# Optimization experiments

Hardware: AMD Instinct MI355X
Metric: run time of the kernel (lower is better)

Reference implementation:

```python
import jax, jax.numpy as jnp
import numpy as np

B, S, H, T = 64, 512, 768, 3


def setup_inputs() -> dict:
    key = jax.random.key(0)
    ks = jax.random.split(key, 8)
    hidden = jax.random.normal(ks[0], (B, S, H), dtype=jnp.float32)
    labels = jax.random.randint(ks[1], (B, S), 0, T, dtype=jnp.int32)
    # variable-length attention mask; torchcrf requires mask[:, 0] all on
    lengths = jax.random.randint(ks[2], (B,), S // 4, S + 1, dtype=jnp.int32)
    mask = (jnp.arange(S)[None, :] < lengths[:, None]).astype(jnp.int32)
    W = jax.random.normal(ks[3], (H, T), dtype=jnp.float32) * 0.02
    b = jax.random.normal(ks[4], (T,), dtype=jnp.float32) * 0.02
    transitions = jax.random.normal(ks[5], (T, T), dtype=jnp.float32) * 0.1
    start_trans = jax.random.normal(ks[6], (T,), dtype=jnp.float32) * 0.1
    end_trans = jax.random.normal(ks[7], (T,), dtype=jnp.float32) * 0.1
    return {"hidden": hidden, "labels": labels, "mask": mask, "W": W, "b": b,
            "transitions": transitions, "start_trans": start_trans, "end_trans": end_trans}


def _crf_nll(emissions, tags, mask, trans, start, end):
    # emissions: (B,S,T) float; tags/mask: (B,S) int. Returns sum NLL (scalar).
    mask_f = mask.astype(emissions.dtype)
    bidx = jnp.arange(emissions.shape[0])
    # --- numerator: score of the given tag path ---
    first_tag = tags[:, 0]
    num = start[first_tag] + emissions[bidx, 0, first_tag]
    prev, cur = tags[:, :-1], tags[:, 1:]
    step = trans[prev, cur] + jnp.take_along_axis(emissions[:, 1:], cur[..., None], axis=2)[..., 0]
    num = num + jnp.sum(step * mask_f[:, 1:], axis=1)
    lengths = jnp.sum(mask, axis=1)
    last_tag = jnp.take_along_axis(tags, (lengths - 1)[:, None], axis=1)[:, 0]
    num = num + end[last_tag]
    # --- denominator: log-partition via forward algorithm (lax.scan) ---
    alpha0 = start[None, :] + emissions[:, 0]  # (B,T)
    def fwd_step(alpha, inp):
        e, m = inp  # e: (B,T), m: (B,)
        nxt = jax.scipy.special.logsumexp(alpha[:, :, None] + trans[None] + e[:, None, :], axis=1)
        return jnp.where(m[:, None] > 0, nxt, alpha), None
    emis_t = jnp.swapaxes(emissions[:, 1:], 0, 1)  # (S-1,B,T)
    mask_t = jnp.swapaxes(mask[:, 1:], 0, 1)       # (S-1,B)
    alpha, _ = jax.lax.scan(fwd_step, alpha0, (emis_t, mask_t))
    logZ = jax.scipy.special.logsumexp(alpha + end[None, :], axis=1)
    return jnp.sum(logZ - num)


def reference(hidden, labels, mask, W, b, transitions, start_trans, end_trans):
    # classifier: Linear + ReLU -> emissions (B,S,T)
    emissions = jax.nn.relu(jnp.einsum("bsh,ht->bst", hidden, W) + b)
    negloglike = _crf_nll(emissions, labels, mask, transitions, start_trans, end_trans)
    return emissions, negloglike
```

## Files before the change

### kernel.cpp

```cpp
#include <hip/hip_runtime.h>
#include <math.h>

#define NB 64
#define NS 512
#define NH 768
#define NT 3
#define EMIS_N (NB * NS * NT)
#define NEGINF (-1e30f)
#define PSTRIDE 12
#define BPB 32

__device__ __forceinline__ float lse3(float a, float b, float c) {
    float m = fmaxf(fmaxf(a, b), c);
    return m + __logf(__expf(a - m) + __expf(b - m) + __expf(c - m));
}

__global__ __launch_bounds__(256) void emis_crf_kernel(
    const float* __restrict__ hidden,
    const int*   __restrict__ labels,
    const int*   __restrict__ mask,
    const float* __restrict__ W,
    const float* __restrict__ bias,
    const float* __restrict__ trans,
    const float* __restrict__ startv,
    float* __restrict__ out,
    float* __restrict__ ws)
{
    __shared__ float sP[4][12];

    const int tid  = threadIdx.x;
    const int lane = tid & 63;
    const int wv   = tid >> 6;
    const int wid  = blockIdx.x * 4 + wv;
    const int sub  = lane & 15;
    const int rsel = lane >> 4;
    const int row  = wid * 4 + rsel;
    const int b    = row >> 9;
    const int p    = row & (NS - 1);

    if (blockIdx.x == 0 && tid == 0) out[EMIS_N] = 0.0f;

    const int* lrow = labels + b * NS;
    const int* mrow = mask   + b * NS;
    int mk = 0, labc = 0, labp = 0;
    if (sub == 0) {
        mk   = mrow[p];
        labc = lrow[p];
        labp = lrow[p - (p > 0 ? 1 : 0)];
    }

    const float* hrow = hidden + (size_t)row * NH;
    float a0 = 0.f, a1 = 0.f, a2 = 0.f;
    #pragma unroll
    for (int it = 0; it < 12; ++it) {
        const int h0 = it * 64 + sub * 4;
        const float4 x  = *reinterpret_cast<const float4*>(hrow + h0);
        const float4 q0 = *reinterpret_cast<const float4*>(W + h0 * 3);
        const float4 q1 = *reinterpret_cast<const float4*>(W + h0 * 3 + 4);
        const float4 q2 = *reinterpret_cast<const float4*>(W + h0 * 3 + 8);
        a0 = fmaf(x.x, q0.x, a0); a1 = fmaf(x.x, q0.y, a1); a2 = fmaf(x.x, q0.z, a2);
        a0 = fmaf(x.y, q0.w, a0); a1 = fmaf(x.y, q1.x, a1); a2 = fmaf(x.y, q1.y, a2);
        a0 = fmaf(x.z, q1.z, a0); a1 = fmaf(x.z, q1.w, a1); a2 = fmaf(x.z, q2.x, a2);
        a0 = fmaf(x.w, q2.y, a0); a1 = fmaf(x.w, q2.z, a1); a2 = fmaf(x.w, q2.w, a2);
    }
    #pragma unroll
    for (int d = 8; d; d >>= 1) {
        a0 += __shfl_xor(a0, d);
        a1 += __shfl_xor(a1, d);
        a2 += __shfl_xor(a2, d);
    }

    const float e0 = fmaxf(a0 + bias[0], 0.f);
    const float e1 = fmaxf(a1 + bias[1], 0.f);
    const float e2 = fmaxf(a2 + bias[2], 0.f);

    if (sub < 3) out[row * NT + sub] = (sub == 0) ? e0 : (sub == 1) ? e1 : e2;

    float term = 0.f;
    if (sub == 0) {
        const float esel = (labc == 0) ? e0 : (labc == 1) ? e1 : e2;
        if (p == 0) {
            term = startv[labc] + esel;
        } else if (mk) {
            term = trans[labp * 3 + labc] + esel;
        }
    }

    const int il = (lane < 9) ? (lane / 3) : 0;
    const int jl = (lane < 9) ? (lane % 3) : 0;
    const float tc0 = trans[jl], tc1 = trans[3 + jl], tc2 = trans[6 + jl];
    float Pv = (il == jl) ? 0.f : NEGINF;

    const int pbase = p & ~3;
    #pragma unroll
    for (int k = 0; k < 4; ++k) {
        const int src = k << 4;
        const float ee0 = __shfl(e0, src);
        const float ee1 = __shfl(e1, src);
        const float ee2 = __shfl(e2, src);
        const int   mm  = __shfl(mk, src);
        const float Pi0 = __shfl(Pv, il * 3 + 0);
        const float Pi1 = __shfl(Pv, il * 3 + 1);
        const float Pi2 = __shfl(Pv, il * 3 + 2);
        const float ej  = (jl == 0) ? ee0 : (jl == 1) ? ee1 : ee2;
        const float q   = lse3(Pi0 + tc0, Pi1 + tc1, Pi2 + tc2) + ej;
        const bool act  = ((pbase + k) >= 1) && (mm != 0);
        Pv = act ? q : Pv;
    }

    const float np = __shfl(term, 0) + __shfl(term, 16) +
                     __shfl(term, 32) + __shfl(term, 48);

    if (lane < 9)  sP[wv][lane] = Pv;
    if (lane == 0) sP[wv][9]    = np;
    __syncthreads();
    if (wv == 0) {
        float Pb = (lane < 9) ? sP[0][lane] : 0.f;
        #pragma unroll
        for (int k = 1; k < 4; ++k) {
            const float Pi0 = __shfl(Pb, il * 3 + 0);
            const float Pi1 = __shfl(Pb, il * 3 + 1);
            const float Pi2 = __shfl(Pb, il * 3 + 2);
            const float q = lse3(Pi0 + sP[k][jl],
                                 Pi1 + sP[k][3 + jl],
                                 Pi2 + sP[k][6 + jl]);
            Pb = (lane < 9) ? q : Pb;
        }
        float* wp = ws + blockIdx.x * PSTRIDE;
        if (lane < 9)  wp[lane] = Pb;
        if (lane == 0) wp[9] = sP[0][9] + sP[1][9] + sP[2][9] + sP[3][9];
    }
}

__global__ __launch_bounds__(64) void crf_combine(
    const float* __restrict__ emis,
    const int*   __restrict__ labels,
    const int*   __restrict__ mask,
    const float* __restrict__ startv,
    const float* __restrict__ endv,
    const float* __restrict__ ws,
    float* __restrict__ nll)
{
    const int b    = blockIdx.x;
    const int lane = threadIdx.x;

    float P[9] = {0.f, NEGINF, NEGINF, NEGINF, 0.f, NEGINF, NEGINF, NEGINF, 0.f};
    float np = 0.f;
    if (lane < BPB) {
        const float* pa = ws + ((size_t)b * BPB + lane) * PSTRIDE;
        #pragma unroll
        for (int i = 0; i < 9; ++i) P[i] = pa[i];
        np = pa[9];
    }

    const int* mrow = mask   + b * NS;
    const int* lrow = labels + b * NS;
    int lsum = 0;
    #pragma unroll
    for (int k = 0; k < 8; ++k) lsum += mrow[lane + k * 64];
    #pragma unroll
    for (int d = 32; d; d >>= 1) lsum += __shfl_xor(lsum, d);
    const int len = lsum;

    #pragma unroll
    for (int d = 1; d < BPB; d <<= 1) {
        float Q[9];
        #pragma unroll
        for (int i = 0; i < 9; ++i) Q[i] = __shfl_down(P[i], d);
        const bool valid = (lane + d) < BPB;
        float R[9];
        #pragma unroll
        for (int i = 0; i < 3; ++i)
            #pragma unroll
            for (int j = 0; j < 3; ++j)
                R[i * 3 + j] = lse3(P[i * 3 + 0] + Q[0 + j],
                                    P[i * 3 + 1] + Q[3 + j],
                                    P[i * 3 + 2] + Q[6 + j]);
        #pragma unroll
        for (int i = 0; i < 9; ++i) P[i] = valid ? R[i] : P[i];
    }

    #pragma unroll
    for (int d = 32; d; d >>= 1) np += __shfl_xor(np, d);

    if (lane == 0) {
        const float* erow = emis + (size_t)b * NS * NT;
        const float a0 = startv[0] + erow[0];
        const float a1 = startv[1] + erow[1];
        const float a2 = startv[2] + erow[2];
        const float f0 = lse3(a0 + P[0], a1 + P[3], a2 + P[6]);
        const float f1 = lse3(a0 + P[1], a1 + P[4], a2 + P[7]);
        const float f2 = lse3(a0 + P[2], a1 + P[5], a2 + P[8]);
        const float logZ = lse3(f0 + endv[0], f1 + endv[1], f2 + endv[2]);

        const int tl = lrow[len - 1];
        const float num = np + endv[tl];
        atomicAdd(nll, logZ - num);
    }
}

extern "C" void kernel_launch(void* const* d_in, const int* in_sizes, int n_in,
                              void* d_out, int out_size, void* d_ws, size_t ws_size,
                              hipStream_t stream) {
    const float* hidden = (const float*)d_in[0];
    const int*   labels = (const int*)  d_in[1];
    const int*   maskp  = (const int*)  d_in[2];
    const float* W      = (const float*)d_in[3];
    const float* bias   = (const float*)d_in[4];
    const float* trans  = (const float*)d_in[5];
    const float* startv = (const float*)d_in[6];
    const float* endv   = (const float*)d_in[7];
    float* out = (float*)d_out;
    float* ws  = (float*)d_ws;

    emis_crf_kernel<<<2048, 256, 0, stream>>>(hidden, labels, maskp, W, bias,
                                              trans, startv, out, ws);
    crf_combine<<<NB, 64, 0, stream>>>(out, labels, maskp, startv, endv, ws,
                                       out + EMIS_N);
}
```

Baseline: 28.89 us.

## Fuse CRF combine into emission kernel via last-block atomic tickets

Merges the two-kernel pipeline into one launch. Each block publishes its partial transfer matrix with atomics and bumps a per-sequence ticket. The last block to finish for a sequence runs the scan combine, and a global ticket lets the last sequence do the final NLL sum deterministically. This removes a kernel launch and the gap between launches, but adds a memset launch, atomic traffic and fences.

After: 44.08 us. 52.6% more time.

```diff
diff --git a/kernel.cpp b/kernel.cpp
--- a/kernel.cpp
+++ b/kernel.cpp
@@ -7,15 +7,18 @@
 #define NT 3
 #define EMIS_N (NB * NS * NT)
 #define NEGINF (-1e30f)
-#define PSTRIDE 12
+#define PSTRIDE 16
 #define BPB 32
+#define NBLK 2048
 
 __device__ __forceinline__ float lse3(float a, float b, float c) {
     float m = fmaxf(fmaxf(a, b), c);
     return m + __logf(__expf(a - m) + __expf(b - m) + __expf(c - m));
 }
 
-__global__ __launch_bounds__(256) void emis_crf_kernel(
+__device__ __forceinline__ float aread(float* p) { return atomicAdd(p, 0.0f); }
+
+__global__ __launch_bounds__(256) void fused_emis_crf(
     const float* __restrict__ hidden,
     const int*   __restrict__ labels,
     const int*   __restrict__ mask,
@@ -23,22 +26,26 @@
     const float* __restrict__ bias,
     const float* __restrict__ trans,
     const float* __restrict__ startv,
+    const float* __restrict__ endv,
     float* __restrict__ out,
-    float* __restrict__ ws)
+    float* __restrict__ partials,
+    float* __restrict__ nslots,
+    unsigned int* __restrict__ btick,
+    unsigned int* __restrict__ ftick)
 {
     __shared__ float sP[4][12];
+    __shared__ float sE[3];
 
     const int tid  = threadIdx.x;
     const int lane = tid & 63;
     const int wv   = tid >> 6;
-    const int wid  = blockIdx.x * 4 + wv;
+    const int blk  = blockIdx.x;
+    const int wid  = blk * 4 + wv;
     const int sub  = lane & 15;
     const int rsel = lane >> 4;
     const int row  = wid * 4 + rsel;
     const int b    = row >> 9;
     const int p    = row & (NS - 1);
-
-    if (blockIdx.x == 0 && tid == 0) out[EMIS_N] = 0.0f;
 
     const int* lrow = labels + b * NS;
     const int* mrow = mask   + b * NS;
@@ -113,48 +120,46 @@
 
     if (lane < 9)  sP[wv][lane] = Pv;
     if (lane == 0) sP[wv][9]    = np;
+    if ((blk & (BPB - 1)) == 0 && wv == 0 && lane == 0) {
+        sE[0] = e0; sE[1] = e1; sE[2] = e2;
+    }
     __syncthreads();
-    if (wv == 0) {
-        float Pb = (lane < 9) ? sP[0][lane] : 0.f;
-        #pragma unroll
-        for (int k = 1; k < 4; ++k) {
-            const float Pi0 = __shfl(Pb, il * 3 + 0);
-            const float Pi1 = __shfl(Pb, il * 3 + 1);
-            const float Pi2 = __shfl(Pb, il * 3 + 2);
-            const float q = lse3(Pi0 + sP[k][jl],
-                                 Pi1 + sP[k][3 + jl],
-                                 Pi2 + sP[k][6 + jl]);
-            Pb = (lane < 9) ? q : Pb;
-        }
-        float* wp = ws + blockIdx.x * PSTRIDE;
-        if (lane < 9)  wp[lane] = Pb;
-        if (lane == 0) wp[9] = sP[0][9] + sP[1][9] + sP[2][9] + sP[3][9];
-    }
-}
-
-__global__ __launch_bounds__(64) void crf_combine(
-    const float* __restrict__ emis,
-    const int*   __restrict__ labels,
-    const int*   __restrict__ mask,
-    const float* __restrict__ startv,
-    const float* __restrict__ endv,
-    const float* __restrict__ ws,
-    float* __restrict__ nll)
-{
-    const int b    = blockIdx.x;
-    const int lane = threadIdx.x;
+    if (wv != 0) return;
+
+    float Pb = (lane < 9) ? sP[0][lane] : 0.f;
+    #pragma unroll
+    for (int k = 1; k < 4; ++k) {
+        const float Pi0 = __shfl(Pb, il * 3 + 0);
+        const float Pi1 = __shfl(Pb, il * 3 + 1);
+        const float Pi2 = __shfl(Pb, il * 3 + 2);
+        const float q = lse3(Pi0 + sP[k][jl],
+                             Pi1 + sP[k][3 + jl],
+                             Pi2 + sP[k][6 + jl]);
+        Pb = (lane < 9) ? q : Pb;
+    }
+    const float npb = sP[0][9] + sP[1][9] + sP[2][9] + sP[3][9];
+
+    float* wp = partials + (size_t)blk * PSTRIDE;
+    if (lane < 9)  atomicExch(wp + lane, Pb);
+    if (lane == 9) atomicExch(wp + 9, npb);
+    if ((blk & (BPB - 1)) == 0 && lane >= 10 && lane < 13)
+        atomicExch(wp + lane, sE[lane - 10]);
+    asm volatile("s_waitcnt vmcnt(0)" ::: "memory");
+
+    unsigned int old = 0u;
+    if (lane == 0) old = atomicAdd(btick + b, 1u);
+    old = (unsigned int)__shfl((int)old, 0);
+    if (old != (BPB - 1u)) return;
 
     float P[9] = {0.f, NEGINF, NEGINF, NEGINF, 0.f, NEGINF, NEGINF, NEGINF, 0.f};
-    float np = 0.f;
+    float np2 = 0.f;
     if (lane < BPB) {
-        const float* pa = ws + ((size_t)b * BPB + lane) * PSTRIDE;
-        #pragma unroll
-        for (int i = 0; i < 9; ++i) P[i] = pa[i];
-        np = pa[9];
-    }
-
-    const int* mrow = mask   + b * NS;
-    const int* lrow = labels + b * NS;
+        float* pa = partials + ((size_t)b * BPB + lane) * PSTRIDE;
+        #pragma unroll
+        for (int i = 0; i < 9; ++i) P[i] = aread(pa + i);
+        np2 = aread(pa + 9);
+    }
+
     int lsum = 0;
     #pragma unroll
     for (int k = 0; k < 8; ++k) lsum += mrow[lane + k * 64];
@@ -181,22 +186,34 @@
     }
 
     #pragma unroll
-    for (int d = 32; d; d >>= 1) np += __shfl_xor(np, d);
+    for (int d = 32; d; d >>= 1) np2 += __shfl_xor(np2, d);
 
     if (lane == 0) {
-        const float* erow = emis + (size_t)b * NS * NT;
-        const float a0 = startv[0] + erow[0];
-        const float a1 = startv[1] + erow[1];
-        const float a2 = startv[2] + erow[2];
-        const float f0 = lse3(a0 + P[0], a1 + P[3], a2 + P[6]);
-        const float f1 = lse3(a0 + P[1], a1 + P[4], a2 + P[7]);
-        const float f2 = lse3(a0 + P[2], a1 + P[5], a2 + P[8]);
+        float* pa0 = partials + (size_t)b * BPB * PSTRIDE;
+        const float ae0 = aread(pa0 + 10);
+        const float ae1 = aread(pa0 + 11);
+        const float ae2 = aread(pa0 + 12);
+        const float b0 = startv[0] + ae0;
+        const float b1 = startv[1] + ae1;
+        const float b2 = startv[2] + ae2;
+        const float f0 = lse3(b0 + P[0], b1 + P[3], b2 + P[6]);
+        const float f1 = lse3(b0 + P[1], b1 + P[4], b2 + P[7]);
+        const float f2 = lse3(b0 + P[2], b1 + P[5], b2 + P[8]);
         const float logZ = lse3(f0 + endv[0], f1 + endv[1], f2 + endv[2]);
-
         const int tl = lrow[len - 1];
-        const float num = np + endv[tl];
-        atomicAdd(nll, logZ - num);
-    }
+        atomicExch(nslots + b, logZ - (np2 + endv[tl]));
+    }
+    asm volatile("s_waitcnt vmcnt(0)" ::: "memory");
+
+    unsigned int o2 = 0u;
+    if (lane == 0) o2 = atomicAdd(ftick, 1u);
+    o2 = (unsigned int)__shfl((int)o2, 0);
+    if (o2 != (NB - 1u)) return;
+
+    float v = aread(nslots + lane);
+    #pragma unroll
+    for (int d = 32; d; d >>= 1) v += __shfl_xor(v, d);
+    if (lane == 0) out[EMIS_N] = v;
 }
 
 extern "C" void kernel_launch(void* const* d_in, const int* in_sizes, int n_in,
@@ -211,10 +228,15 @@
     const float* startv = (const float*)d_in[6];
     const float* endv   = (const float*)d_in[7];
     float* out = (float*)d_out;
-    float* ws  = (float*)d_ws;
-
-    emis_crf_kernel<<<2048, 256, 0, stream>>>(hidden, labels, maskp, W, bias,
-                                              trans, startv, out, ws);
-    crf_combine<<<NB, 64, 0, stream>>>(out, labels, maskp, startv, endv, ws,
-                                       out + EMIS_N);
+
+    float*        partials = (float*)d_ws;
+    float*        nslots   = partials + NBLK * PSTRIDE;
+    unsigned int* btick    = (unsigned int*)(nslots + NB);
+    unsigned int* ftick    = btick + NB;
+
+    hipMemsetAsync(btick, 0, (NB + 1) * sizeof(unsigned int), stream);
+
+    fused_emis_crf<<<NBLK, 256, 0, stream>>>(hidden, labels, maskp, W, bias,
+                                             trans, startv, endv, out,
+                                             partials, nslots, btick, ftick);
 }
```
